# Kernel tuning notes

Hardware: AMD Instinct MI355X
Metric: run time of the kernel (lower is better)

Reference implementation:

```python
import jax, jax.numpy as jnp
import numpy as np
import math

B, L, F, R = 64, 16, 64, 1023


def setup_inputs() -> dict:
    key = jax.random.key(0)
    ks = jax.random.split(key, 12)

    def prob(k):
        p = jax.random.uniform(k, (B, L), dtype=jnp.float32) + 1e-3
        return p / p.sum(-1, keepdims=True)  # sparsemax-style simplex weights

    x = jax.random.normal(ks[0], (B, L, F, R), dtype=jnp.float32)
    car_w = prob(ks[1])
    cdr_w = prob(ks[2])
    cons1_w = prob(ks[3])
    cons2_w = prob(ks[4])
    root_filler = jax.random.normal(ks[5], (B, F), dtype=jnp.float32)
    s = 0.05
    D_l = jax.random.normal(ks[6], (R, R), dtype=jnp.float32) * s
    D_r = jax.random.normal(ks[7], (R, R), dtype=jnp.float32) * s
    E_l = jax.random.normal(ks[8], (R, R), dtype=jnp.float32) * s
    E_r = jax.random.normal(ks[9], (R, R), dtype=jnp.float32) * s
    root_role = jax.random.normal(ks[10], (R,), dtype=jnp.float32)
    return dict(x=x, car_w=car_w, cdr_w=cdr_w, cons1_w=cons1_w, cons2_w=cons2_w,
                root_filler=root_filler, D_l=D_l, D_r=D_r, E_l=E_l, E_r=E_r,
                root_role=root_role)


def _entropy(p):
    # torch.distributions.Categorical(p).entropy() / log(num_cats)
    return -(p * jnp.log(p + 1e-12)).sum(-1) / math.log(p.shape[-1])


def reference(x, car_w, cdr_w, cons1_w, cons2_w, root_filler, D_l, D_r, E_l, E_r, root_role):
    # --- CarNet (dense branch, empty_filler_initialization != 'random') ---
    car_arg = jnp.einsum('blfr,bl->bfr', x, car_w)          # weighted memory read
    car_out = jnp.einsum('bfr,tr->bft', car_arg, D_l)       # left-child extraction
    # --- CdrNet ---
    cdr_arg = jnp.einsum('blfr,bl->bfr', x, cdr_w)
    cdr_out = jnp.einsum('bfr,tr->bft', cdr_arg, D_r)       # right-child extraction
    # --- ConsNet ---
    c1 = jnp.einsum('blfr,bl->bfr', x, cons1_w)
    c2 = jnp.einsum('blfr,bl->bfr', x, cons2_w)
    cons_out = (jnp.einsum('bfr,tr->bft', c1, E_l)
                + jnp.einsum('bfr,tr->bft', c2, E_r)
                + root_filler[:, :, None] * root_role[None, None, :])
    ents = (_entropy(car_w), _entropy(cdr_w), _entropy(cons1_w), _entropy(cons2_w))
    maxes = (car_w.max(1), cdr_w.max(1), cons1_w.max(1), cons2_w.max(1))
    return (car_out, cdr_out, cons_out) + ents + maxes
```

## Files before the change

### kernel.cpp

```cpp
#include <hip/hip_runtime.h>
#include <hip/hip_bf16.h>
#include <stdint.h>

#define Rdim 1023
#define BFR  4190208

typedef __bf16 bf16;
typedef __bf16 bf16x8 __attribute__((ext_vector_type(8)));
typedef __bf16 bf16x4 __attribute__((ext_vector_type(4)));
typedef float  f32x4  __attribute__((ext_vector_type(4)));
typedef float  f32x4u __attribute__((ext_vector_type(4), aligned(4)));

__device__ __forceinline__ void async16(const void* g, void* l) {
    __builtin_amdgcn_global_load_lds(
        (const __attribute__((address_space(1))) void*)g,
        (__attribute__((address_space(3))) void*)l, 16, 0, 0);
}

#define BAR()  do { __builtin_amdgcn_s_barrier(); __builtin_amdgcn_sched_barrier(0); } while(0)

__global__ __launch_bounds__(256) void k_prep(
    const float* __restrict__ x,
    const float* __restrict__ w0, const float* __restrict__ w1,
    const float* __restrict__ w2, const float* __restrict__ w3,
    const float* __restrict__ Dl, const float* __restrict__ Dr,
    const float* __restrict__ El, const float* __restrict__ Er,
    bf16* __restrict__ args, bf16* __restrict__ dpad,
    float* __restrict__ out)
{
    const int blk = blockIdx.x;
    const int t   = threadIdx.x;

    if (blk < 4096) {
        const int b = blk >> 6;
        float wr0[16], wr1[16], wr2[16], wr3[16];
#pragma unroll
        for (int l = 0; l < 16; ++l) {
            wr0[l] = w0[b*16 + l]; wr1[l] = w1[b*16 + l];
            wr2[l] = w2[b*16 + l]; wr3[l] = w3[b*16 + l];
        }
        const float* xb = x + ((size_t)(b*16)*64 + (blk & 63)) * (size_t)Rdim;
        float a0[4] = {}, a1[4] = {}, a2[4] = {}, a3[4] = {};
        if (t < 255) {
#pragma unroll
            for (int l = 0; l < 16; ++l) {
                f32x4u v = *(const f32x4u*)(xb + (size_t)l*(64*(size_t)Rdim) + t*4);
#pragma unroll
                for (int j = 0; j < 4; ++j) {
                    a0[j] += wr0[l]*v[j]; a1[j] += wr1[l]*v[j];
                    a2[j] += wr2[l]*v[j]; a3[j] += wr3[l]*v[j];
                }
            }
        } else {
#pragma unroll
            for (int l = 0; l < 16; ++l) {
                const float* p = xb + (size_t)l*(64*(size_t)Rdim) + 1020;
#pragma unroll
                for (int j = 0; j < 3; ++j) {
                    float v = p[j];
                    a0[j] += wr0[l]*v; a1[j] += wr1[l]*v;
                    a2[j] += wr2[l]*v; a3[j] += wr3[l]*v;
                }
            }
        }
        const int c   = t >> 1;
        const int S2  = (blk >> 1) & 3;
        const int cw  = (c & ~3) | ((c & 3) ^ S2);
        const int off = (cw << 3) + ((t & 1) << 2);
        bf16x4 s0, s1, s2, s3;
#pragma unroll
        for (int j = 0; j < 4; ++j) {
            s0[j] = (bf16)a0[j]; s1[j] = (bf16)a1[j];
            s2[j] = (bf16)a2[j]; s3[j] = (bf16)a3[j];
        }
        *(bf16x4*)(args +            (size_t)blk*1024 + off) = s0;
        *(bf16x4*)(args + 4194304 +  (size_t)blk*1024 + off) = s1;
        bf16* c12 = args + 8388608 + (size_t)blk*2048;
        *(bf16x4*)(c12 + off)        = s2;
        *(bf16x4*)(c12 + 1024 + off) = s3;
    } else if (blk < 6144) {
        const int id = (blk - 4096)*256 + t;
        const float* src; int n, c, K; size_t base;
        if (id < 262144) {
            const int m2  = id >> 17;
            src = m2 ? Dr : Dl;
            const int rem = id & 131071;
            n = rem >> 7; c = rem & 127; K = 1024;
            base = m2 ? 1048576u : 0u;
        } else {
            const int rem = id - 262144;
            n = rem >> 8; c = rem & 255; K = 2048;
            base = 2097152u;
            src = (c < 128) ? El : Er;
        }
        const int cl = c & 127;
        float v[8] = {};
        if (n < Rdim) {
            const float* sp = src + (size_t)n*Rdim + cl*8;
            if (cl < 127) {
                f32x4u u0 = *(const f32x4u*)sp;
                f32x4u u1 = *(const f32x4u*)(sp + 4);
#pragma unroll
                for (int j = 0; j < 4; ++j) { v[j] = u0[j]; v[4+j] = u1[j]; }
            } else {
                f32x4u u0 = *(const f32x4u*)sp;
#pragma unroll
                for (int j = 0; j < 4; ++j) v[j] = u0[j];
                v[4] = sp[4]; v[5] = sp[5]; v[6] = sp[6];
            }
        }
        const int swc = (c & ~3) | ((c & 3) ^ ((n >> 1) & 3));
        bf16x8 s;
#pragma unroll
        for (int j = 0; j < 8; ++j) s[j] = (bf16)v[j];
        *(bf16x8*)(dpad + base + (size_t)n*K + swc*8) = s;
    } else {
        const int k = t >> 6, b2 = t & 63;
        const float* w = (k==0) ? w0 : (k==1) ? w1 : (k==2) ? w2 : w3;
        float s = 0.f, mx = -1e30f;
#pragma unroll
        for (int l = 0; l < 16; ++l) {
            float p = w[b2*16 + l];
            s += p * logf(p + 1e-12f);
            mx = fmaxf(mx, p);
        }
        out[3*(size_t)BFR +       k*64 + b2] = -s / logf(16.f);
        out[3*(size_t)BFR + 256 + k*64 + b2] = mx;
    }
}

template<int BM, int NKT, int VM, bool CONS>
__device__ __forceinline__ void gemm_t(
    const bf16* __restrict__ Ab, const bf16* __restrict__ Bb,
    const float* __restrict__ rf, const float* __restrict__ rr,
    float* __restrict__ outp, char* lds, int mt, int nt)
{
    constexpr int AstB = CONS ? 4096 : 2048;
    constexpr int MI   = BM / 32;
    constexpr int ABUF = BM * 64;

    const int tid  = threadIdx.x;
    const int wave = tid >> 6, lane = tid & 63;
    const int wm   = wave >> 2, wn = wave & 3;
    const int lr   = lane & 15, lk = lane >> 4;
    const int cc16 = (lk ^ ((lr >> 1) & 3)) << 4;

    const char* AgT = (const char*)Ab + (size_t)(mt*BM  + (tid>>2))*AstB + (tid&3)*16;
    const char* BgT = (const char*)Bb + (size_t)(nt*256 + (tid>>2))*AstB + (tid&3)*16;

    f32x4 acc[MI][4] = {};
    bf16x8 af[MI], bfr[4];

#define STG(bufidx, kt) do {                                                  \
    char* _a = lds + (bufidx)*ABUF + wave*1024;                               \
    char* _b = lds + 49152 + (bufidx)*16384 + wave*1024;                      \
    const size_t _ko = (size_t)(kt)*64;                                       \
    _Pragma("unroll") for (int i = 0; i < BM/128; ++i)                        \
        async16(AgT + (size_t)(i*128)*AstB + _ko, _a + i*8192);               \
    _Pragma("unroll") for (int i = 0; i < 2; ++i)                             \
        async16(BgT + (size_t)(i*128)*AstB + _ko, _b + i*8192);               \
} while(0)

    STG(0, 0); STG(1, 1);
    asm volatile("s_waitcnt vmcnt(%0)" :: "n"(VM) : "memory");
    BAR();

    int cb = 0;
    for (int kt = 0; kt < NKT; ++kt) {
        char* cA = lds + cb*ABUF;
        char* cB = lds + 49152 + cb*16384;
        int sb = cb + 2; if (sb >= 3) sb -= 3;
        const bool st = (kt + 2 < NKT);
#pragma unroll
        for (int mi = 0; mi < MI; ++mi)
            af[mi] = *(const bf16x8*)(cA + (wm*(BM/2) + mi*16 + lr)*64 + cc16);
#pragma unroll
        for (int j = 0; j < 4; ++j)
            bfr[j] = *(const bf16x8*)(cB + (wn*64 + j*16 + lr)*64 + cc16);
        if (st) STG(sb, kt+2);
        __builtin_amdgcn_s_setprio(1);
#pragma unroll
        for (int mi = 0; mi < MI; ++mi)
#pragma unroll
        for (int j = 0; j < 4; ++j)
            acc[mi][j] = __builtin_amdgcn_mfma_f32_16x16x32_bf16(
                af[mi], bfr[j], acc[mi][j], 0, 0, 0);
        __builtin_amdgcn_s_setprio(0);
        if (st)                { asm volatile("s_waitcnt vmcnt(%0)" :: "n"(VM) : "memory"); }
        else if (kt == NKT-2)  { asm volatile("s_waitcnt vmcnt(0)" ::: "memory"); }
        BAR();
        cb = cb + 1; if (cb == 3) cb = 0;
    }
#undef STG

#pragma unroll
    for (int mi = 0; mi < MI; ++mi) {
        const int gm0 = mt*BM + wm*(BM/2) + mi*16 + lk*4;
#pragma unroll
        for (int j = 0; j < 4; ++j) {
            const int gn = nt*256 + wn*64 + j*16 + lr;
            if (gn < Rdim) {
                const float rv = CONS ? rr[gn] : 0.f;
#pragma unroll
                for (int q = 0; q < 4; ++q) {
                    float v = acc[mi][j][q];
                    if (CONS) v += rf[gm0 + q] * rv;
                    outp[(size_t)(gm0 + q)*Rdim + gn] = v;
                }
            }
        }
    }
}

__global__ __launch_bounds__(512, 1) void k_gemm(
    const bf16* __restrict__ args, const bf16* __restrict__ dpad,
    const float* __restrict__ root_filler, const float* __restrict__ root_role,
    float* __restrict__ out)
{
    __shared__ char lds[98304];
    const int bid = blockIdx.x;
    const int xcd = bid & 7, idx = bid >> 3;

    if (idx < 16) {
        const int tile = xcd*16 + idx;
        gemm_t<128, 64, 3, true >(args + 8388608, dpad + 2097152,
            root_filler, root_role, out + 2*(size_t)BFR, lds, tile >> 2, tile & 3);
    } else if (idx < 24) {
        const int tile = xcd*8 + idx - 16;
        gemm_t<256, 32, 4, false>(args, dpad,
            root_filler, root_role, out, lds, tile >> 2, tile & 3);
    } else {
        const int tile = xcd*8 + idx - 24;
        gemm_t<256, 32, 4, false>(args + 4194304, dpad + 1048576,
            root_filler, root_role, out + (size_t)BFR, lds, tile >> 2, tile & 3);
    }
}

extern "C" void kernel_launch(void* const* d_in, const int* in_sizes, int n_in,
                              void* d_out, int out_size, void* d_ws, size_t ws_size,
                              hipStream_t stream)
{
    const float* x           = (const float*)d_in[0];
    const float* car_w       = (const float*)d_in[1];
    const float* cdr_w       = (const float*)d_in[2];
    const float* cons1_w     = (const float*)d_in[3];
    const float* cons2_w     = (const float*)d_in[4];
    const float* root_filler = (const float*)d_in[5];
    const float* Dl          = (const float*)d_in[6];
    const float* Dr          = (const float*)d_in[7];
    const float* El          = (const float*)d_in[8];
    const float* Er          = (const float*)d_in[9];
    const float* root_role   = (const float*)d_in[10];
    float* out = (float*)d_out;

    bf16* args = (bf16*)d_ws;
    bf16* dpad = args + 16777216;

    k_prep<<<dim3(6145), dim3(256), 0, stream>>>(
        x, car_w, cdr_w, cons1_w, cons2_w, Dl, Dr, El, Er, args, dpad, out);
    k_gemm<<<dim3(256),  dim3(512), 0, stream>>>(
        args, dpad, root_filler, root_role, out);
}
```

Measured before the change: 107.1 us.

## Stream x reduction through double-buffered async LDS loads in persistent blocks

The weighted memory-read reduction over x moves from 4096 one-shot blocks with direct global loads to 512 persistent blocks. Each block processes 16 half-rows, prefetching the next tile into a double-buffered LDS area with global_load_lds while it reduces the current one. The goal is to hide global memory latency on the dominant 268 MB x read and to cut block launch overhead. In exchange it adds 64 KB of LDS per block, two barriers per step, address clamping at the buffer end, and a special tail path for the last three columns.

```diff
diff --git a/kernel.cpp b/kernel.cpp
--- a/kernel.cpp
+++ b/kernel.cpp
@@ -7,7 +7,7 @@
 
 typedef __bf16 bf16;
 typedef __bf16 bf16x8 __attribute__((ext_vector_type(8)));
-typedef __bf16 bf16x4 __attribute__((ext_vector_type(4)));
+typedef __bf16 bf16x2 __attribute__((ext_vector_type(2)));
 typedef float  f32x4  __attribute__((ext_vector_type(4)));
 typedef float  f32x4u __attribute__((ext_vector_type(4), aligned(4)));
 
@@ -28,58 +28,12 @@
     bf16* __restrict__ args, bf16* __restrict__ dpad,
     float* __restrict__ out)
 {
+    __shared__ char plds[65536];
     const int blk = blockIdx.x;
     const int t   = threadIdx.x;
 
-    if (blk < 4096) {
-        const int b = blk >> 6;
-        float wr0[16], wr1[16], wr2[16], wr3[16];
-#pragma unroll
-        for (int l = 0; l < 16; ++l) {
-            wr0[l] = w0[b*16 + l]; wr1[l] = w1[b*16 + l];
-            wr2[l] = w2[b*16 + l]; wr3[l] = w3[b*16 + l];
-        }
-        const float* xb = x + ((size_t)(b*16)*64 + (blk & 63)) * (size_t)Rdim;
-        float a0[4] = {}, a1[4] = {}, a2[4] = {}, a3[4] = {};
-        if (t < 255) {
-#pragma unroll
-            for (int l = 0; l < 16; ++l) {
-                f32x4u v = *(const f32x4u*)(xb + (size_t)l*(64*(size_t)Rdim) + t*4);
-#pragma unroll
-                for (int j = 0; j < 4; ++j) {
-                    a0[j] += wr0[l]*v[j]; a1[j] += wr1[l]*v[j];
-                    a2[j] += wr2[l]*v[j]; a3[j] += wr3[l]*v[j];
-                }
-            }
-        } else {
-#pragma unroll
-            for (int l = 0; l < 16; ++l) {
-                const float* p = xb + (size_t)l*(64*(size_t)Rdim) + 1020;
-#pragma unroll
-                for (int j = 0; j < 3; ++j) {
-                    float v = p[j];
-                    a0[j] += wr0[l]*v; a1[j] += wr1[l]*v;
-                    a2[j] += wr2[l]*v; a3[j] += wr3[l]*v;
-                }
-            }
-        }
-        const int c   = t >> 1;
-        const int S2  = (blk >> 1) & 3;
-        const int cw  = (c & ~3) | ((c & 3) ^ S2);
-        const int off = (cw << 3) + ((t & 1) << 2);
-        bf16x4 s0, s1, s2, s3;
-#pragma unroll
-        for (int j = 0; j < 4; ++j) {
-            s0[j] = (bf16)a0[j]; s1[j] = (bf16)a1[j];
-            s2[j] = (bf16)a2[j]; s3[j] = (bf16)a3[j];
-        }
-        *(bf16x4*)(args +            (size_t)blk*1024 + off) = s0;
-        *(bf16x4*)(args + 4194304 +  (size_t)blk*1024 + off) = s1;
-        bf16* c12 = args + 8388608 + (size_t)blk*2048;
-        *(bf16x4*)(c12 + off)        = s2;
-        *(bf16x4*)(c12 + 1024 + off) = s3;
-    } else if (blk < 6144) {
-        const int id = (blk - 4096)*256 + t;
+    if (blk < 2048) {
+        const int id = blk*256 + t;
         const float* src; int n, c, K; size_t base;
         if (id < 262144) {
             const int m2  = id >> 17;
@@ -114,7 +68,7 @@
 #pragma unroll
         for (int j = 0; j < 8; ++j) s[j] = (bf16)v[j];
         *(bf16x8*)(dpad + base + (size_t)n*K + swc*8) = s;
-    } else {
+    } else if (blk == 2048) {
         const int k = t >> 6, b2 = t & 63;
         const float* w = (k==0) ? w0 : (k==1) ? w1 : (k==2) ? w2 : w3;
         float s = 0.f, mx = -1e30f;
@@ -126,6 +80,85 @@
         }
         out[3*(size_t)BFR +       k*64 + b2] = -s / logf(16.f);
         out[3*(size_t)BFR + 256 + k*64 + b2] = mx;
+    } else {
+        const int b512 = blk - 2049;
+        const char* xB    = (const char*)x;
+        const char* xlast = xB + (size_t)67043328*4 - 16;
+        const int wv = t >> 6;
+        const int la16 = (t & 63) * 16;
+
+#define PISSUE(STEP, BUF) do {                                                \
+    const int h_ = (STEP)*512 + b512;                                         \
+    const int m_ = h_ >> 1, half_ = h_ & 1;                                   \
+    const size_t rowB_ = (size_t)((m_>>6)*1024 + (m_&63)) * 4092;             \
+    _Pragma("unroll") for (int j = 0; j < 8; ++j) {                           \
+        const int q_ = wv*8 + j, l_ = q_ >> 1, sub_ = q_ & 1;                 \
+        const char* s_ = xB + rowB_ + (size_t)l_*261888                       \
+                            + half_*2048 + sub_*1024 + la16;                  \
+        if (s_ > xlast) s_ = xlast;                                           \
+        async16(s_, plds + (BUF)*32768 + q_*1024);                            \
+    }                                                                         \
+} while(0)
+
+        PISSUE(0, 0);
+        for (int s = 0; s < 16; ++s) {
+            if (s < 15) { PISSUE(s+1, (s+1)&1);
+                          asm volatile("s_waitcnt vmcnt(8)" ::: "memory"); }
+            else        { asm volatile("s_waitcnt vmcnt(0)" ::: "memory"); }
+            BAR();
+            const int h = s*512 + b512, m = h >> 1, half = h & 1;
+            const int bq = m >> 6;
+            float a0[2] = {}, a1[2] = {}, a2[2] = {}, a3[2] = {};
+            const char* bb = plds + (s & 1)*32768;
+#pragma unroll
+            for (int l = 0; l < 16; ++l) {
+                const float2 v = *(const float2*)(bb + l*2048 + t*8);
+                const float u0 = w0[bq*16 + l], u1 = w1[bq*16 + l];
+                const float u2 = w2[bq*16 + l], u3 = w3[bq*16 + l];
+                a0[0] += u0*v.x; a0[1] += u0*v.y;
+                a1[0] += u1*v.x; a1[1] += u1*v.y;
+                a2[0] += u2*v.x; a2[1] += u2*v.y;
+                a3[0] += u3*v.x; a3[1] += u3*v.y;
+            }
+            if (half == 1 && t == 255) {
+                a0[1] = a1[1] = a2[1] = a3[1] = 0.f;
+            }
+            const int r0  = half*512 + t*2;
+            const int c   = r0 >> 3;
+            const int S2  = (m >> 1) & 3;
+            const int off = (((c & ~3) | ((c & 3) ^ S2)) << 3) + (r0 & 7);
+            bf16x2 s0, s1, s2, s3;
+            s0[0] = (bf16)a0[0]; s0[1] = (bf16)a0[1];
+            s1[0] = (bf16)a1[0]; s1[1] = (bf16)a1[1];
+            s2[0] = (bf16)a2[0]; s2[1] = (bf16)a2[1];
+            s3[0] = (bf16)a3[0]; s3[1] = (bf16)a3[1];
+            *(bf16x2*)(args +            (size_t)m*1024 + off) = s0;
+            *(bf16x2*)(args + 4194304 +  (size_t)m*1024 + off) = s1;
+            bf16* c12 = args + 8388608 + (size_t)m*2048;
+            *(bf16x2*)(c12 + off)        = s2;
+            *(bf16x2*)(c12 + 1024 + off) = s3;
+            BAR();
+        }
+#undef PISSUE
+
+        if (b512 == 511 && t < 3) {
+            asm volatile("s_waitcnt vmcnt(0)" ::: "memory");
+            const int r = 1020 + t;
+            float s0 = 0.f, s1 = 0.f, s2 = 0.f, s3 = 0.f;
+#pragma unroll
+            for (int l = 0; l < 16; ++l) {
+                const float xv = x[(size_t)(63*1024 + 63)*1023
+                                   + (size_t)l*65472 + r];
+                s0 += w0[63*16 + l]*xv; s1 += w1[63*16 + l]*xv;
+                s2 += w2[63*16 + l]*xv; s3 += w3[63*16 + l]*xv;
+            }
+            const int off = (124 << 3) + (r & 7);
+            args[(size_t)4095*1024 + off]           = (bf16)s0;
+            args[4194304 + (size_t)4095*1024 + off] = (bf16)s1;
+            bf16* c12 = args + 8388608 + (size_t)4095*2048;
+            c12[off]        = (bf16)s2;
+            c12[1024 + off] = (bf16)s3;
+        }
     }
 }
 
@@ -256,7 +289,7 @@
     bf16* args = (bf16*)d_ws;
     bf16* dpad = args + 16777216;
 
-    k_prep<<<dim3(6145), dim3(256), 0, stream>>>(
+    k_prep<<<dim3(2561), dim3(256), 0, stream>>>(
         x, car_w, cdr_w, cons1_w, cons2_w, Dl, Dr, El, Er, args, dpad, out);
     k_gemm<<<dim3(256),  dim3(512), 0, stream>>>(
         args, dpad, root_filler, root_role, out);
```

Result: no change. 109.1 us (+1.8%).

## Deepen GEMM LDS pipeline to four stages and reorder prep block dispatch

Applied to the files above, without the earlier changes.

The GEMM main loop moves from triple to quadruple buffering in LDS, prefetching three k-tiles ahead with adjusted vmcnt waits, and LDS grows to 128 KB. This is meant to hide more global-load latency behind the MFMA work. The prep kernel also now dispatches the weight-matrix conversion blocks before the x reduction blocks, which changes scheduling order. The larger LDS footprint still fits one block per CU under the existing launch bounds, but the wait-count logic must stay correct at the tail of the loop.

```diff
diff --git a/kernel.cpp b/kernel.cpp
--- a/kernel.cpp
+++ b/kernel.cpp
@@ -31,55 +31,8 @@
     const int blk = blockIdx.x;
     const int t   = threadIdx.x;
 
-    if (blk < 4096) {
-        const int b = blk >> 6;
-        float wr0[16], wr1[16], wr2[16], wr3[16];
-#pragma unroll
-        for (int l = 0; l < 16; ++l) {
-            wr0[l] = w0[b*16 + l]; wr1[l] = w1[b*16 + l];
-            wr2[l] = w2[b*16 + l]; wr3[l] = w3[b*16 + l];
-        }
-        const float* xb = x + ((size_t)(b*16)*64 + (blk & 63)) * (size_t)Rdim;
-        float a0[4] = {}, a1[4] = {}, a2[4] = {}, a3[4] = {};
-        if (t < 255) {
-#pragma unroll
-            for (int l = 0; l < 16; ++l) {
-                f32x4u v = *(const f32x4u*)(xb + (size_t)l*(64*(size_t)Rdim) + t*4);
-#pragma unroll
-                for (int j = 0; j < 4; ++j) {
-                    a0[j] += wr0[l]*v[j]; a1[j] += wr1[l]*v[j];
-                    a2[j] += wr2[l]*v[j]; a3[j] += wr3[l]*v[j];
-                }
-            }
-        } else {
-#pragma unroll
-            for (int l = 0; l < 16; ++l) {
-                const float* p = xb + (size_t)l*(64*(size_t)Rdim) + 1020;
-#pragma unroll
-                for (int j = 0; j < 3; ++j) {
-                    float v = p[j];
-                    a0[j] += wr0[l]*v; a1[j] += wr1[l]*v;
-                    a2[j] += wr2[l]*v; a3[j] += wr3[l]*v;
-                }
-            }
-        }
-        const int c   = t >> 1;
-        const int S2  = (blk >> 1) & 3;
-        const int cw  = (c & ~3) | ((c & 3) ^ S2);
-        const int off = (cw << 3) + ((t & 1) << 2);
-        bf16x4 s0, s1, s2, s3;
-#pragma unroll
-        for (int j = 0; j < 4; ++j) {
-            s0[j] = (bf16)a0[j]; s1[j] = (bf16)a1[j];
-            s2[j] = (bf16)a2[j]; s3[j] = (bf16)a3[j];
-        }
-        *(bf16x4*)(args +            (size_t)blk*1024 + off) = s0;
-        *(bf16x4*)(args + 4194304 +  (size_t)blk*1024 + off) = s1;
-        bf16* c12 = args + 8388608 + (size_t)blk*2048;
-        *(bf16x4*)(c12 + off)        = s2;
-        *(bf16x4*)(c12 + 1024 + off) = s3;
-    } else if (blk < 6144) {
-        const int id = (blk - 4096)*256 + t;
+    if (blk < 2048) {
+        const int id = blk*256 + t;
         const float* src; int n, c, K; size_t base;
         if (id < 262144) {
             const int m2  = id >> 17;
@@ -114,6 +67,54 @@
 #pragma unroll
         for (int j = 0; j < 8; ++j) s[j] = (bf16)v[j];
         *(bf16x8*)(dpad + base + (size_t)n*K + swc*8) = s;
+    } else if (blk < 6144) {
+        const int m = blk - 2048;
+        const int b = m >> 6;
+        float wr0[16], wr1[16], wr2[16], wr3[16];
+#pragma unroll
+        for (int l = 0; l < 16; ++l) {
+            wr0[l] = w0[b*16 + l]; wr1[l] = w1[b*16 + l];
+            wr2[l] = w2[b*16 + l]; wr3[l] = w3[b*16 + l];
+        }
+        const float* xb = x + ((size_t)(b*16)*64 + (m & 63)) * (size_t)Rdim;
+        float a0[4] = {}, a1[4] = {}, a2[4] = {}, a3[4] = {};
+        if (t < 255) {
+#pragma unroll
+            for (int l = 0; l < 16; ++l) {
+                f32x4u v = *(const f32x4u*)(xb + (size_t)l*(64*(size_t)Rdim) + t*4);
+#pragma unroll
+                for (int j = 0; j < 4; ++j) {
+                    a0[j] += wr0[l]*v[j]; a1[j] += wr1[l]*v[j];
+                    a2[j] += wr2[l]*v[j]; a3[j] += wr3[l]*v[j];
+                }
+            }
+        } else {
+#pragma unroll
+            for (int l = 0; l < 16; ++l) {
+                const float* p = xb + (size_t)l*(64*(size_t)Rdim) + 1020;
+#pragma unroll
+                for (int j = 0; j < 3; ++j) {
+                    float v = p[j];
+                    a0[j] += wr0[l]*v; a1[j] += wr1[l]*v;
+                    a2[j] += wr2[l]*v; a3[j] += wr3[l]*v;
+                }
+            }
+        }
+        const int c   = t >> 1;
+        const int S2  = (m >> 1) & 3;
+        const int cw  = (c & ~3) | ((c & 3) ^ S2);
+        const int off = (cw << 3) + ((t & 1) << 2);
+        bf16x4 s0, s1, s2, s3;
+#pragma unroll
+        for (int j = 0; j < 4; ++j) {
+            s0[j] = (bf16)a0[j]; s1[j] = (bf16)a1[j];
+            s2[j] = (bf16)a2[j]; s3[j] = (bf16)a3[j];
+        }
+        *(bf16x4*)(args +            (size_t)m*1024 + off) = s0;
+        *(bf16x4*)(args + 4194304 +  (size_t)m*1024 + off) = s1;
+        bf16* c12 = args + 8388608 + (size_t)m*2048;
+        *(bf16x4*)(c12 + off)        = s2;
+        *(bf16x4*)(c12 + 1024 + off) = s3;
     } else {
         const int k = t >> 6, b2 = t & 63;
         const float* w = (k==0) ? w0 : (k==1) ? w1 : (k==2) ? w2 : w3;
@@ -129,7 +130,7 @@
     }
 }
 
-template<int BM, int NKT, int VM, bool CONS>
+template<int BM, int NKT, bool CONS>
 __device__ __forceinline__ void gemm_t(
     const bf16* __restrict__ Ab, const bf16* __restrict__ Bb,
     const float* __restrict__ rf, const float* __restrict__ rr,
@@ -138,6 +139,7 @@
     constexpr int AstB = CONS ? 4096 : 2048;
     constexpr int MI   = BM / 32;
     constexpr int ABUF = BM * 64;
+    constexpr int U    = BM/128 + 2;
 
     const int tid  = threadIdx.x;
     const int wave = tid >> 6, lane = tid & 63;
@@ -153,7 +155,7 @@
 
 #define STG(bufidx, kt) do {                                                  \
     char* _a = lds + (bufidx)*ABUF + wave*1024;                               \
-    char* _b = lds + 49152 + (bufidx)*16384 + wave*1024;                      \
+    char* _b = lds + 65536 + (bufidx)*16384 + wave*1024;                      \
     const size_t _ko = (size_t)(kt)*64;                                       \
     _Pragma("unroll") for (int i = 0; i < BM/128; ++i)                        \
         async16(AgT + (size_t)(i*128)*AstB + _ko, _a + i*8192);               \
@@ -161,23 +163,23 @@
         async16(BgT + (size_t)(i*128)*AstB + _ko, _b + i*8192);               \
 } while(0)
 
-    STG(0, 0); STG(1, 1);
-    asm volatile("s_waitcnt vmcnt(%0)" :: "n"(VM) : "memory");
+    STG(0, 0); STG(1, 1); STG(2, 2);
+    asm volatile("s_waitcnt vmcnt(%0)" :: "n"(2*U) : "memory");
     BAR();
 
     int cb = 0;
     for (int kt = 0; kt < NKT; ++kt) {
         char* cA = lds + cb*ABUF;
-        char* cB = lds + 49152 + cb*16384;
-        int sb = cb + 2; if (sb >= 3) sb -= 3;
-        const bool st = (kt + 2 < NKT);
+        char* cB = lds + 65536 + cb*16384;
+        const int sb = (cb + 3) & 3;
+        const bool st = (kt + 3 < NKT);
 #pragma unroll
         for (int mi = 0; mi < MI; ++mi)
             af[mi] = *(const bf16x8*)(cA + (wm*(BM/2) + mi*16 + lr)*64 + cc16);
 #pragma unroll
         for (int j = 0; j < 4; ++j)
             bfr[j] = *(const bf16x8*)(cB + (wn*64 + j*16 + lr)*64 + cc16);
-        if (st) STG(sb, kt+2);
+        if (st) STG(sb, kt+3);
         __builtin_amdgcn_s_setprio(1);
 #pragma unroll
         for (int mi = 0; mi < MI; ++mi)
@@ -186,10 +188,11 @@
             acc[mi][j] = __builtin_amdgcn_mfma_f32_16x16x32_bf16(
                 af[mi], bfr[j], acc[mi][j], 0, 0, 0);
         __builtin_amdgcn_s_setprio(0);
-        if (st)                { asm volatile("s_waitcnt vmcnt(%0)" :: "n"(VM) : "memory"); }
-        else if (kt == NKT-2)  { asm volatile("s_waitcnt vmcnt(0)" ::: "memory"); }
+        if (st)                 { asm volatile("s_waitcnt vmcnt(%0)" :: "n"(2*U) : "memory"); }
+        else if (kt == NKT-3)   { asm volatile("s_waitcnt vmcnt(%0)" :: "n"(U)   : "memory"); }
+        else if (kt == NKT-2)   { asm volatile("s_waitcnt vmcnt(0)" ::: "memory"); }
         BAR();
-        cb = cb + 1; if (cb == 3) cb = 0;
+        cb = (cb + 1) & 3;
     }
 #undef STG
 
@@ -217,21 +220,21 @@
     const float* __restrict__ root_filler, const float* __restrict__ root_role,
     float* __restrict__ out)
 {
-    __shared__ char lds[98304];
+    __shared__ char lds[131072];
     const int bid = blockIdx.x;
     const int xcd = bid & 7, idx = bid >> 3;
 
     if (idx < 16) {
         const int tile = xcd*16 + idx;
-        gemm_t<128, 64, 3, true >(args + 8388608, dpad + 2097152,
+        gemm_t<128, 64, true >(args + 8388608, dpad + 2097152,
             root_filler, root_role, out + 2*(size_t)BFR, lds, tile >> 2, tile & 3);
     } else if (idx < 24) {
         const int tile = xcd*8 + idx - 16;
-        gemm_t<256, 32, 4, false>(args, dpad,
+        gemm_t<256, 32, false>(args, dpad,
             root_filler, root_role, out, lds, tile >> 2, tile & 3);
     } else {
         const int tile = xcd*8 + idx - 24;
-        gemm_t<256, 32, 4, false>(args + 4194304, dpad + 1048576,
+        gemm_t<256, 32, false>(args + 4194304, dpad + 1048576,
             root_filler, root_role, out + (size_t)BFR, lds, tile >> 2, tile & 3);
     }
 }
```

Result: slower. 110.3 us (+3.0%).

## Switch GEMM operands from bf16 to fp8 e4m3 with scaled weights

Applied to the files above, without the earlier changes.

Converts the weighted-sum activations and the R×R extraction matrices to fp8 e4m3 instead of bf16, with the weights pre-scaled by 16 and the result rescaled by 1/16. The GEMM now uses the fp8 MFMA with two k-substeps per 64-byte LDS row and half the K-tiles, and the prep kernel is reordered so the weight conversion blocks come first. This halves workspace traffic and the number of staged tiles but costs a large loss in precision that may exceed the tolerance.

```diff
diff --git a/kernel.cpp b/kernel.cpp
--- a/kernel.cpp
+++ b/kernel.cpp
@@ -1,13 +1,11 @@
 #include <hip/hip_runtime.h>
 #include <hip/hip_bf16.h>
+#include <hip/hip_fp8.h>
 #include <stdint.h>
 
 #define Rdim 1023
 #define BFR  4190208
 
-typedef __bf16 bf16;
-typedef __bf16 bf16x8 __attribute__((ext_vector_type(8)));
-typedef __bf16 bf16x4 __attribute__((ext_vector_type(4)));
 typedef float  f32x4  __attribute__((ext_vector_type(4)));
 typedef float  f32x4u __attribute__((ext_vector_type(4), aligned(4)));
 
@@ -18,6 +16,14 @@
 }
 
 #define BAR()  do { __builtin_amdgcn_s_barrier(); __builtin_amdgcn_sched_barrier(0); } while(0)
+
+__device__ __forceinline__ uint32_t f2fp8(float f) {
+    __hip_fp8_e4m3 v(f);
+    return (uint32_t)v.__x;
+}
+__device__ __forceinline__ uint32_t pack4(const float* a, float s) {
+    return f2fp8(s*a[0]) | (f2fp8(s*a[1])<<8) | (f2fp8(s*a[2])<<16) | (f2fp8(s*a[3])<<24);
+}
 
 __global__ __launch_bounds__(256) void k_prep(
     const float* __restrict__ x,
@@ -25,21 +31,64 @@
     const float* __restrict__ w2, const float* __restrict__ w3,
     const float* __restrict__ Dl, const float* __restrict__ Dr,
     const float* __restrict__ El, const float* __restrict__ Er,
-    bf16* __restrict__ args, bf16* __restrict__ dpad,
+    uint8_t* __restrict__ args8, uint8_t* __restrict__ dpad8,
     float* __restrict__ out)
 {
     const int blk = blockIdx.x;
     const int t   = threadIdx.x;
 
-    if (blk < 4096) {
-        const int b = blk >> 6;
+    if (blk < 1024) {
+        const int id = blk*256 + t;
+        const float* src; int n, c16, r0; size_t dst; int stride;
+        if (id < 131072) {
+            const int mat = id >> 16;
+            src = mat ? Dr : Dl;
+            const int rem = id & 65535;
+            n = rem >> 6; c16 = rem & 63; r0 = c16*16; stride = 1024;
+            dst = (mat ? 1048576u : 0u);
+        } else {
+            const int rem = id - 131072;
+            n = rem >> 7; c16 = rem & 127;
+            r0 = (c16 & 63)*16; stride = 2048;
+            src = (c16 < 64) ? El : Er;
+            dst = 2097152u;
+        }
+        const int pos = ((c16 >> 2) << 6) + (((c16 & 3) ^ ((n >> 1) & 3)) << 4);
+        float v[16] = {};
+        if (n < Rdim) {
+            const float* sp = src + (size_t)n*Rdim + r0;
+            if (r0 <= Rdim - 16) {
+#pragma unroll
+                for (int j = 0; j < 4; ++j) {
+                    f32x4u u = *(const f32x4u*)(sp + j*4);
+#pragma unroll
+                    for (int q = 0; q < 4; ++q) v[j*4+q] = u[q];
+                }
+            } else {
+#pragma unroll
+                for (int j = 0; j < 3; ++j) {
+                    f32x4u u = *(const f32x4u*)(sp + j*4);
+#pragma unroll
+                    for (int q = 0; q < 4; ++q) v[j*4+q] = u[q];
+                }
+                v[12] = sp[12]; v[13] = sp[13]; v[14] = sp[14];
+            }
+        }
+        uint32_t w[4];
+#pragma unroll
+        for (int j = 0; j < 4; ++j) w[j] = pack4(v + j*4, 16.f);
+        *(uint4*)(dpad8 + dst + (size_t)n*stride + pos) =
+            make_uint4(w[0], w[1], w[2], w[3]);
+    } else if (blk < 5120) {
+        const int m = blk - 1024;
+        const int b = m >> 6;
         float wr0[16], wr1[16], wr2[16], wr3[16];
 #pragma unroll
         for (int l = 0; l < 16; ++l) {
             wr0[l] = w0[b*16 + l]; wr1[l] = w1[b*16 + l];
             wr2[l] = w2[b*16 + l]; wr3[l] = w3[b*16 + l];
         }
-        const float* xb = x + ((size_t)(b*16)*64 + (blk & 63)) * (size_t)Rdim;
+        const float* xb = x + ((size_t)(b*16)*64 + (m & 63)) * (size_t)Rdim;
         float a0[4] = {}, a1[4] = {}, a2[4] = {}, a3[4] = {};
         if (t < 255) {
 #pragma unroll
@@ -63,57 +112,14 @@
                 }
             }
         }
-        const int c   = t >> 1;
-        const int S2  = (blk >> 1) & 3;
-        const int cw  = (c & ~3) | ((c & 3) ^ S2);
-        const int off = (cw << 3) + ((t & 1) << 2);
-        bf16x4 s0, s1, s2, s3;
-#pragma unroll
-        for (int j = 0; j < 4; ++j) {
-            s0[j] = (bf16)a0[j]; s1[j] = (bf16)a1[j];
-            s2[j] = (bf16)a2[j]; s3[j] = (bf16)a3[j];
-        }
-        *(bf16x4*)(args +            (size_t)blk*1024 + off) = s0;
-        *(bf16x4*)(args + 4194304 +  (size_t)blk*1024 + off) = s1;
-        bf16* c12 = args + 8388608 + (size_t)blk*2048;
-        *(bf16x4*)(c12 + off)        = s2;
-        *(bf16x4*)(c12 + 1024 + off) = s3;
-    } else if (blk < 6144) {
-        const int id = (blk - 4096)*256 + t;
-        const float* src; int n, c, K; size_t base;
-        if (id < 262144) {
-            const int m2  = id >> 17;
-            src = m2 ? Dr : Dl;
-            const int rem = id & 131071;
-            n = rem >> 7; c = rem & 127; K = 1024;
-            base = m2 ? 1048576u : 0u;
-        } else {
-            const int rem = id - 262144;
-            n = rem >> 8; c = rem & 255; K = 2048;
-            base = 2097152u;
-            src = (c < 128) ? El : Er;
-        }
-        const int cl = c & 127;
-        float v[8] = {};
-        if (n < Rdim) {
-            const float* sp = src + (size_t)n*Rdim + cl*8;
-            if (cl < 127) {
-                f32x4u u0 = *(const f32x4u*)sp;
-                f32x4u u1 = *(const f32x4u*)(sp + 4);
-#pragma unroll
-                for (int j = 0; j < 4; ++j) { v[j] = u0[j]; v[4+j] = u1[j]; }
-            } else {
-                f32x4u u0 = *(const f32x4u*)sp;
-#pragma unroll
-                for (int j = 0; j < 4; ++j) v[j] = u0[j];
-                v[4] = sp[4]; v[5] = sp[5]; v[6] = sp[6];
-            }
-        }
-        const int swc = (c & ~3) | ((c & 3) ^ ((n >> 1) & 3));
-        bf16x8 s;
-#pragma unroll
-        for (int j = 0; j < 8; ++j) s[j] = (bf16)v[j];
-        *(bf16x8*)(dpad + base + (size_t)n*K + swc*8) = s;
+        const int r0  = t*4;
+        const int S2  = (m >> 1) & 3;
+        const int pos = ((r0 >> 6) << 6) + ((((r0 >> 4) & 3) ^ S2) << 4) + (r0 & 15);
+        *(uint32_t*)(args8 +            (size_t)m*1024 + pos) = pack4(a0, 1.f);
+        *(uint32_t*)(args8 + 4194304 +  (size_t)m*1024 + pos) = pack4(a1, 1.f);
+        uint8_t* c12 = args8 + 8388608 + (size_t)m*2048;
+        *(uint32_t*)(c12 + pos)        = pack4(a2, 1.f);
+        *(uint32_t*)(c12 + 1024 + pos) = pack4(a3, 1.f);
     } else {
         const int k = t >> 6, b2 = t & 63;
         const float* w = (k==0) ? w0 : (k==1) ? w1 : (k==2) ? w2 : w3;
@@ -131,11 +137,11 @@
 
 template<int BM, int NKT, int VM, bool CONS>
 __device__ __forceinline__ void gemm_t(
-    const bf16* __restrict__ Ab, const bf16* __restrict__ Bb,
+    const uint8_t* __restrict__ Ab, const uint8_t* __restrict__ Bb,
     const float* __restrict__ rf, const float* __restrict__ rr,
     float* __restrict__ outp, char* lds, int mt, int nt)
 {
-    constexpr int AstB = CONS ? 4096 : 2048;
+    constexpr int AstB = CONS ? 2048 : 1024;
     constexpr int MI   = BM / 32;
     constexpr int ABUF = BM * 64;
 
@@ -143,13 +149,15 @@
     const int wave = tid >> 6, lane = tid & 63;
     const int wm   = wave >> 2, wn = wave & 3;
     const int lr   = lane & 15, lk = lane >> 4;
-    const int cc16 = (lk ^ ((lr >> 1) & 3)) << 4;
-
-    const char* AgT = (const char*)Ab + (size_t)(mt*BM  + (tid>>2))*AstB + (tid&3)*16;
-    const char* BgT = (const char*)Bb + (size_t)(nt*256 + (tid>>2))*AstB + (tid&3)*16;
+    const int sw   = (lr >> 1) & 3;
+    const int cb0 = ((((lk >> 1)    ) ^ sw) << 4) + ((lk & 1) << 3);
+    const int cb1 = (((2 + (lk >> 1)) ^ sw) << 4) + ((lk & 1) << 3);
+
+    const uint8_t* AgT = Ab + (size_t)(mt*BM  + (tid>>2))*AstB + (tid&3)*16;
+    const uint8_t* BgT = Bb + (size_t)(nt*256 + (tid>>2))*AstB + (tid&3)*16;
 
     f32x4 acc[MI][4] = {};
-    bf16x8 af[MI], bfr[4];
+    long af[MI][2], bfr[4][2];
 
 #define STG(bufidx, kt) do {                                                  \
     char* _a = lds + (bufidx)*ABUF + wave*1024;                               \
@@ -172,19 +180,27 @@
         int sb = cb + 2; if (sb >= 3) sb -= 3;
         const bool st = (kt + 2 < NKT);
 #pragma unroll
-        for (int mi = 0; mi < MI; ++mi)
-            af[mi] = *(const bf16x8*)(cA + (wm*(BM/2) + mi*16 + lr)*64 + cc16);
-#pragma unroll
-        for (int j = 0; j < 4; ++j)
-            bfr[j] = *(const bf16x8*)(cB + (wn*64 + j*16 + lr)*64 + cc16);
+        for (int mi = 0; mi < MI; ++mi) {
+            const char* rp = cA + (wm*(BM/2) + mi*16 + lr)*64;
+            af[mi][0] = *(const long*)(rp + cb0);
+            af[mi][1] = *(const long*)(rp + cb1);
+        }
+#pragma unroll
+        for (int j = 0; j < 4; ++j) {
+            const char* rp = cB + (wn*64 + j*16 + lr)*64;
+            bfr[j][0] = *(const long*)(rp + cb0);
+            bfr[j][1] = *(const long*)(rp + cb1);
+        }
         if (st) STG(sb, kt+2);
         __builtin_amdgcn_s_setprio(1);
 #pragma unroll
+        for (int ks = 0; ks < 2; ++ks)
+#pragma unroll
         for (int mi = 0; mi < MI; ++mi)
 #pragma unroll
         for (int j = 0; j < 4; ++j)
-            acc[mi][j] = __builtin_amdgcn_mfma_f32_16x16x32_bf16(
-                af[mi], bfr[j], acc[mi][j], 0, 0, 0);
+            acc[mi][j] = __builtin_amdgcn_mfma_f32_16x16x32_fp8_fp8(
+                af[mi][ks], bfr[j][ks], acc[mi][j], 0, 0, 0);
         __builtin_amdgcn_s_setprio(0);
         if (st)                { asm volatile("s_waitcnt vmcnt(%0)" :: "n"(VM) : "memory"); }
         else if (kt == NKT-2)  { asm volatile("s_waitcnt vmcnt(0)" ::: "memory"); }
@@ -203,7 +219,7 @@
                 const float rv = CONS ? rr[gn] : 0.f;
 #pragma unroll
                 for (int q = 0; q < 4; ++q) {
-                    float v = acc[mi][j][q];
+                    float v = acc[mi][j][q] * 0.0625f;
                     if (CONS) v += rf[gm0 + q] * rv;
                     outp[(size_t)(gm0 + q)*Rdim + gn] = v;
                 }
@@ -213,7 +229,7 @@
 }
 
 __global__ __launch_bounds__(512, 1) void k_gemm(
-    const bf16* __restrict__ args, const bf16* __restrict__ dpad,
+    const uint8_t* __restrict__ args8, const uint8_t* __restrict__ dpad8,
     const float* __restrict__ root_filler, const float* __restrict__ root_role,
     float* __restrict__ out)
 {
@@ -223,15 +239,15 @@
 
     if (idx < 16) {
         const int tile = xcd*16 + idx;
-        gemm_t<128, 64, 3, true >(args + 8388608, dpad + 2097152,
+        gemm_t<128, 32, 3, true >(args8 + 8388608, dpad8 + 2097152,
             root_filler, root_role, out + 2*(size_t)BFR, lds, tile >> 2, tile & 3);
     } else if (idx < 24) {
         const int tile = xcd*8 + idx - 16;
-        gemm_t<256, 32, 4, false>(args, dpad,
+        gemm_t<256, 16, 4, false>(args8, dpad8,
             root_filler, root_role, out, lds, tile >> 2, tile & 3);
     } else {
         const int tile = xcd*8 + idx - 24;
-        gemm_t<256, 32, 4, false>(args + 4194304, dpad + 1048576,
+        gemm_t<256, 16, 4, false>(args8 + 4194304, dpad8 + 1048576,
             root_filler, root_role, out + (size_t)BFR, lds, tile >> 2, tile & 3);
     }
 }
@@ -253,11 +269,11 @@
     const float* root_role   = (const float*)d_in[10];
     float* out = (float*)d_out;
 
-    bf16* args = (bf16*)d_ws;
-    bf16* dpad = args + 16777216;
-
-    k_prep<<<dim3(6145), dim3(256), 0, stream>>>(
-        x, car_w, cdr_w, cons1_w, cons2_w, Dl, Dr, El, Er, args, dpad, out);
+    uint8_t* args8 = (uint8_t*)d_ws;
+    uint8_t* dpad8 = args8 + 16777216;
+
+    k_prep<<<dim3(5121), dim3(256), 0, stream>>>(
+        x, car_w, cdr_w, cons1_w, cons2_w, Dl, Dr, El, Er, args8, dpad8, out);
     k_gemm<<<dim3(256),  dim3(512), 0, stream>>>(
-        args, dpad, root_filler, root_role, out);
-}
+        args8, dpad8, root_filler, root_role, out);
+}
```

Measured after the change: 102.7 us. 4.2% less time.
